# Kernel optimization log

Hardware: AMD Instinct MI355X
Metric: run time of the kernel (lower is better)

Reference implementation:

```python
import jax, jax.numpy as jnp
import numpy as np

HEADS = 16
HEAD_DIM = 64
EMBED = HEADS * HEAD_DIM  # 1024
N, L = 4, 4096


def setup_inputs() -> dict:
    key = jax.random.key(0)
    k1, k2, k3, k4, k5, k6, k7, k8 = jax.random.split(key, 8)
    s = 0.02
    return {
        "q": jax.random.normal(k1, (N, L, EMBED), jnp.float32),
        "k": jax.random.normal(k2, (N, L, EMBED), jnp.float32),
        "v": jax.random.normal(k3, (N, L, EMBED), jnp.float32),
        "mask": jnp.ones((N, L, HEADS, HEADS), jnp.int32),
        # torch Linear weights: (out_features, in_features)
        "q_w": jax.random.normal(k4, (HEAD_DIM, HEAD_DIM), jnp.float32) * s,
        "k_w": jax.random.normal(k5, (HEAD_DIM, HEAD_DIM), jnp.float32) * s,
        "v_w": jax.random.normal(k6, (HEAD_DIM, HEAD_DIM), jnp.float32) * s,
        "fc_w": jax.random.normal(k7, (EMBED, EMBED), jnp.float32) * s,
        "fc_b": jax.random.normal(k8, (EMBED,), jnp.float32) * s,
    }


def reference(q, k, v, mask, q_w, k_w, v_w, fc_w, fc_b):
    n, ql = q.shape[0], q.shape[1]
    # reshape to (N, L, H, D) and apply per-head-dim linear projections (x @ W.T)
    q4 = q.reshape(n, ql, HEADS, HEAD_DIM) @ q_w.T
    k4 = k.reshape(n, k.shape[1], HEADS, HEAD_DIM) @ k_w.T
    v4 = v.reshape(n, v.shape[1], HEADS, HEAD_DIM) @ v_w.T
    # Faithful to the original: matmul broadcasts over (N, L), contracting head_dim,
    # so logits are (N, L, H, H) -- attention across heads per token.
    scale = 1.0 / jnp.sqrt(jnp.float32(HEAD_DIM))
    logits = jnp.einsum("nlhd,nlgd->nlhg", q4, k4) * scale
    logits = jnp.where(mask == 0, -jnp.inf, logits)
    weights = jax.nn.softmax(logits, axis=-1)
    out4 = jnp.einsum("nlhg,nlgd->nlhd", weights, v4)  # (N, L, H, D)
    # Faithful scrambled reshape: permute to (N, H, L, D) then flatten to (N, L, H*D)
    out = out4.transpose(0, 2, 1, 3).reshape(n, ql, HEADS * HEAD_DIM)
    return out @ fc_w.T + fc_b
```

## Files before the change

kernel.cpp:

```cpp
#include <hip/hip_runtime.h>
#include <hip/hip_bf16.h>
#include <stdint.h>

#define TOKENS 16384
#define LSEQ 4096
#define WPAD 72

typedef short bf16x8 __attribute__((ext_vector_type(8)));
typedef float f32x4 __attribute__((ext_vector_type(4)));

typedef __attribute__((address_space(1))) void as1_t;
typedef __attribute__((address_space(3))) void as3_t;

__device__ __forceinline__ unsigned short f2bf(float x) {
  __hip_bfloat16 t = __float2bfloat16(x);
  return *reinterpret_cast<unsigned short*>(&t);
}

__device__ __forceinline__ void async16(const void* g, void* lds) {
  __builtin_amdgcn_global_load_lds((as1_t*)const_cast<void*>(g),
                                   (as3_t*)lds, 16, 0, 0);
}

__global__ __launch_bounds__(256) void cvt_bf16(const float* __restrict__ s,
                                                unsigned short* __restrict__ d,
                                                int n4) {
  int i = blockIdx.x * 256 + threadIdx.x;
  if (i < n4) {
    float4 f = ((const float4*)s)[i];
    union { unsigned short us[4]; uint2 u2; } pk;
    pk.us[0] = f2bf(f.x); pk.us[1] = f2bf(f.y);
    pk.us[2] = f2bf(f.z); pk.us[3] = f2bf(f.w);
    ((uint2*)d)[i] = pk.u2;
  }
}

__global__ __launch_bounds__(1024) void prep_weights(
    const float* __restrict__ qw, const float* __restrict__ kw,
    const float* __restrict__ vw, unsigned short* __restrict__ Mout,
    unsigned short* __restrict__ vwout) {
  __shared__ float ql[4096], kl[4096];
  const int t = threadIdx.x;
  ((float4*)ql)[t] = ((const float4*)qw)[t];
  ((float4*)kl)[t] = ((const float4*)kw)[t];
  {
    float4 f = ((const float4*)vw)[t];
    union { unsigned short us[4]; uint2 u2; } pk;
    pk.us[0] = f2bf(f.x); pk.us[1] = f2bf(f.y);
    pk.us[2] = f2bf(f.z); pk.us[3] = f2bf(f.w);
    ((uint2*)vwout)[t] = pk.u2;
  }
  __syncthreads();
  const int f = t >> 4;
  const int e0 = (t & 15) * 4;
  float acc0 = 0.f, acc1 = 0.f, acc2 = 0.f, acc3 = 0.f;
#pragma unroll 8
  for (int d = 0; d < 64; ++d) {
    const float qv = ql[d * 64 + f];
    const float4 kv = *(const float4*)&kl[d * 64 + e0];
    acc0 += qv * kv.x; acc1 += qv * kv.y; acc2 += qv * kv.z; acc3 += qv * kv.w;
  }
  union { unsigned short us[4]; uint2 u2; } pk;
  pk.us[0] = f2bf(acc0); pk.us[1] = f2bf(acc1);
  pk.us[2] = f2bf(acc2); pk.us[3] = f2bf(acc3);
  *(uint2*)&Mout[f * 64 + e0] = pk.u2;
}

__global__ __launch_bounds__(256) void attn6(
    const float* __restrict__ q, const float* __restrict__ k,
    const float* __restrict__ v, const int* __restrict__ mask,
    const unsigned short* __restrict__ Mg, const unsigned short* __restrict__ vwg,
    unsigned short* __restrict__ X) {
  __shared__ unsigned short Ml[64 * WPAD];
  __shared__ unsigned short Vw[64 * WPAD];
  __shared__ char stg_[4][6144];
  __shared__ char scr_[4][2048];

  const int tid = threadIdx.x;
  const int l = tid & 63, w = tid >> 6;
  const int lr = l & 15, lg = l >> 4;
  char* stg = stg_[w];
  char* scr = scr_[w];

  {
    const int row = tid >> 2, c0 = (tid & 3) * 16;
    *(uint4*)&Ml[row * WPAD + c0]     = *(const uint4*)(Mg + row * 64 + c0);
    *(uint4*)&Ml[row * WPAD + c0 + 8] = *(const uint4*)(Mg + row * 64 + c0 + 8);
    *(uint4*)&Vw[row * WPAD + c0]     = *(const uint4*)(vwg + row * 64 + c0);
    *(uint4*)&Vw[row * WPAD + c0 + 8] = *(const uint4*)(vwg + row * 64 + c0 + 8);
  }

  const int tok0 = blockIdx.x * 32 + w * 8;

  float4 L[2][12];
  int4 mk[2];
  {
    const size_t tb = (size_t)tok0 * 1024;
#pragma unroll
    for (int i = 0; i < 4; ++i) {
      L[0][i]     = *(const float4*)(q + tb + i * 256 + l * 4);
      L[0][4 + i] = *(const float4*)(k + tb + i * 256 + l * 4);
      L[0][8 + i] = *(const float4*)(v + tb + i * 256 + l * 4);
    }
    mk[0] = *(const int4*)(mask + (size_t)tok0 * 256 + lr * 16 + lg * 4);
  }
  __syncthreads();

  const int fr0 = lr * 128 + ((lg * 16) ^ ((lr & 7) << 4));
  const int fr1 = lr * 128 + (((64 + lg * 16)) ^ ((lr & 7) << 4));

#pragma unroll
  for (int t = 0; t < 8; ++t) {
    const int cur = t & 1, nxt = cur ^ 1;
    const int tok = tok0 + t;

#pragma unroll
    for (int i = 0; i < 4; ++i) {
      const int row = i * 4 + (l >> 4);
      const int cb = (l & 15) * 8;
      char* base = stg + row * 128 + (cb ^ ((row & 7) << 4));
      union { unsigned short us[4]; uint2 u2; } pq, pk_, pv_;
      const float4 fq = L[cur][i], fk = L[cur][4 + i], fv = L[cur][8 + i];
      pq.us[0] = f2bf(fq.x); pq.us[1] = f2bf(fq.y); pq.us[2] = f2bf(fq.z); pq.us[3] = f2bf(fq.w);
      pk_.us[0] = f2bf(fk.x); pk_.us[1] = f2bf(fk.y); pk_.us[2] = f2bf(fk.z); pk_.us[3] = f2bf(fk.w);
      pv_.us[0] = f2bf(fv.x); pv_.us[1] = f2bf(fv.y); pv_.us[2] = f2bf(fv.z); pv_.us[3] = f2bf(fv.w);
      *(uint2*)(base)        = pq.u2;
      *(uint2*)(base + 2048) = pk_.u2;
      *(uint2*)(base + 4096) = pv_.u2;
    }

    if (t < 7) {
      const size_t tb = (size_t)(tok + 1) * 1024;
#pragma unroll
      for (int i = 0; i < 4; ++i) {
        L[nxt][i]     = *(const float4*)(q + tb + i * 256 + l * 4);
        L[nxt][4 + i] = *(const float4*)(k + tb + i * 256 + l * 4);
        L[nxt][8 + i] = *(const float4*)(v + tb + i * 256 + l * 4);
      }
      mk[nxt] = *(const int4*)(mask + (size_t)(tok + 1) * 256 + lr * 16 + lg * 4);
    }
    __builtin_amdgcn_sched_barrier(0);

    const bf16x8 aq0 = *(const bf16x8*)(stg + fr0);
    const bf16x8 aq1 = *(const bf16x8*)(stg + fr1);
    const bf16x8 ak0 = *(const bf16x8*)(stg + 2048 + fr0);
    const bf16x8 ak1 = *(const bf16x8*)(stg + 2048 + fr1);
    const bf16x8 av0 = *(const bf16x8*)(stg + 4096 + fr0);
    const bf16x8 av1 = *(const bf16x8*)(stg + 4096 + fr1);

    f32x4 accu[4], accv[4];
#pragma unroll
    for (int n = 0; n < 4; ++n) {
      const int wrow = (n * 16 + lr) * WPAD;
      f32x4 z = {};
      const bf16x8 bm0 = *(const bf16x8*)&Ml[wrow + lg * 8];
      const bf16x8 bm1 = *(const bf16x8*)&Ml[wrow + 32 + lg * 8];
      accu[n] = __builtin_amdgcn_mfma_f32_16x16x32_bf16(ak0, bm0, z, 0, 0, 0);
      accu[n] = __builtin_amdgcn_mfma_f32_16x16x32_bf16(ak1, bm1, accu[n], 0, 0, 0);
      const bf16x8 bw0 = *(const bf16x8*)&Vw[wrow + lg * 8];
      const bf16x8 bw1 = *(const bf16x8*)&Vw[wrow + 32 + lg * 8];
      accv[n] = __builtin_amdgcn_mfma_f32_16x16x32_bf16(av0, bw0, z, 0, 0, 0);
      accv[n] = __builtin_amdgcn_mfma_f32_16x16x32_bf16(av1, bw1, accv[n], 0, 0, 0);
    }

#pragma unroll
    for (int n = 0; n < 4; ++n)
#pragma unroll
      for (int r = 0; r < 4; ++r) {
        const int row = lg * 4 + r;
        *(unsigned short*)(scr + row * 128 + ((32 * n + 2 * lr) ^ ((row & 7) << 4))) =
            f2bf(accu[n][r]);
      }
    const bf16x8 ua0 = *(const bf16x8*)(scr + fr0);
    const bf16x8 ua1 = *(const bf16x8*)(scr + fr1);
    f32x4 z4 = {};
    f32x4 st = __builtin_amdgcn_mfma_f32_16x16x32_bf16(ua0, aq0, z4, 0, 0, 0);
    st = __builtin_amdgcn_mfma_f32_16x16x32_bf16(ua1, aq1, st, 0, 0, 0);

    float e[4];
    float sm = 0.f;
    const int mks[4] = {mk[cur].x, mk[cur].y, mk[cur].z, mk[cur].w};
#pragma unroll
    for (int r = 0; r < 4; ++r) {
      e[r] = (mks[r] != 0) ? __expf(st[r] * 0.125f) : 0.f;
      sm += e[r];
    }
    sm += __shfl_xor(sm, 16);
    sm += __shfl_xor(sm, 32);
    const float inv = 1.0f / sm;
#pragma unroll
    for (int r = 0; r < 4; ++r) e[r] *= inv;

    bf16x8 apv;
#pragma unroll
    for (int j = 0; j < 8; ++j) {
      const int srcg = (lg * 2 + (j >> 2)) & 3;
      const float pv = __shfl(e[j & 3], lr + srcg * 16, 64);
      apv[j] = (short)((lg < 2) ? f2bf(pv) : (unsigned short)0);
    }

    const int s0 = lr + ((lg & 1) * 2) * 16;
    const int s1 = s0 + 16;
    f32x4 o[4];
#pragma unroll
    for (int n = 0; n < 4; ++n) {
      bf16x8 bv;
#pragma unroll
      for (int j = 0; j < 8; ++j) {
        const float xv = __shfl(accv[n][j & 3], (j < 4) ? s0 : s1, 64);
        bv[j] = (short)f2bf(xv);
      }
      f32x4 z = {};
      o[n] = __builtin_amdgcn_mfma_f32_16x16x32_bf16(apv, bv, z, 0, 0, 0);
    }

#pragma unroll
    for (int n = 0; n < 4; ++n)
#pragma unroll
      for (int r = 0; r < 4; ++r) {
        const int row = lg * 4 + r;
        *(unsigned short*)(scr + row * 128 + ((32 * n + 2 * lr) ^ ((row & 7) << 4))) =
            f2bf(o[n][r]);
      }
    const int nb = tok >> 12, lpos = tok & (LSEQ - 1);
#pragma unroll
    for (int it = 0; it < 2; ++it) {
      const int idx = it * 64 + l;
      const int h = idx >> 3, c = idx & 7;
      const uint4 val = *(const uint4*)(scr + h * 128 + ((c * 16) ^ ((h & 7) << 4)));
      *(uint4*)&X[((size_t)(nb * 16 + h) * LSEQ + lpos) * 64 + c * 8] = val;
    }
  }
}

__global__ __launch_bounds__(256) void gemm_fc(const unsigned short* __restrict__ A,
                                               const unsigned short* __restrict__ B,
                                               const float* __restrict__ bias,
                                               float* __restrict__ C) {
  __shared__ unsigned short sA[128 * 32];
  __shared__ unsigned short sB[128 * 32];
  const int tid = threadIdx.x;
  const int l = tid & 63, w = tid >> 6;
  const int wr = w >> 1, wc = w & 1;

  const int bid = blockIdx.x;
  const int wg = (bid & 7) * 128 + (bid >> 3);
  const int tm = (wg >> 3) * 128;
  const int tn = (wg & 7) * 128;

  f32x4 acc[4][4] = {};

  const int r0 = w * 16 + (l >> 2);
  const int c8 = (l & 3) * 8;

  for (int kt = 0; kt < 32; ++kt) {
    const int k0 = kt * 32;
#pragma unroll
    for (int s = 0; s < 2; ++s) {
      async16(A + (size_t)(tm + s * 64 + r0) * 1024 + k0 + c8,
              (char*)sA + s * 4096 + w * 1024);
      async16(B + (size_t)(tn + s * 64 + r0) * 1024 + k0 + c8,
              (char*)sB + s * 4096 + w * 1024);
    }
    __syncthreads();

    bf16x8 af[4], bfr[4];
#pragma unroll
    for (int fi = 0; fi < 4; ++fi)
      af[fi] = *(const bf16x8*)((const char*)sA +
                                (wr * 64 + fi * 16 + (l & 15)) * 64 + (l >> 4) * 16);
#pragma unroll
    for (int fj = 0; fj < 4; ++fj)
      bfr[fj] = *(const bf16x8*)((const char*)sB +
                                 (wc * 64 + fj * 16 + (l & 15)) * 64 + (l >> 4) * 16);
#pragma unroll
    for (int fi = 0; fi < 4; ++fi)
#pragma unroll
      for (int fj = 0; fj < 4; ++fj)
        acc[fi][fj] = __builtin_amdgcn_mfma_f32_16x16x32_bf16(af[fi], bfr[fj],
                                                              acc[fi][fj], 0, 0, 0);
    __syncthreads();
  }

#pragma unroll
  for (int fj = 0; fj < 4; ++fj) {
    const int col = tn + wc * 64 + fj * 16 + (l & 15);
    const float bv = bias[col];
#pragma unroll
    for (int fi = 0; fi < 4; ++fi) {
#pragma unroll
      for (int r = 0; r < 4; ++r) {
        const int row = tm + wr * 64 + fi * 16 + (l >> 4) * 4 + r;
        C[(size_t)row * 1024 + col] = acc[fi][fj][r] + bv;
      }
    }
  }
}

extern "C" void kernel_launch(void* const* d_in, const int* in_sizes, int n_in,
                              void* d_out, int out_size, void* d_ws, size_t ws_size,
                              hipStream_t stream) {
  (void)in_sizes; (void)n_in; (void)out_size; (void)ws_size;
  const float* q   = (const float*)d_in[0];
  const float* k   = (const float*)d_in[1];
  const float* v   = (const float*)d_in[2];
  const int*  mask = (const int*)d_in[3];
  const float* qw  = (const float*)d_in[4];
  const float* kw  = (const float*)d_in[5];
  const float* vw  = (const float*)d_in[6];
  const float* fcw = (const float*)d_in[7];
  const float* fcb = (const float*)d_in[8];
  float* out = (float*)d_out;

  unsigned short* X   = (unsigned short*)d_ws;
  unsigned short* Wb  = X + (size_t)16 * 1024 * 1024;
  unsigned short* Mw  = Wb + (size_t)1024 * 1024;
  unsigned short* vwb = Mw + 4096;

  cvt_bf16<<<dim3(1024), dim3(256), 0, stream>>>(fcw, Wb, 262144);
  prep_weights<<<dim3(1), dim3(1024), 0, stream>>>(qw, kw, vw, Mw, vwb);
  attn6<<<dim3(512), dim3(256), 0, stream>>>(q, k, v, mask, Mw, vwb, X);
  gemm_fc<<<dim3(1024), dim3(256), 0, stream>>>(X, Wb, fcb, out);
}
```

Measured before the change: 116.8 us.

## Stream attention inputs via async global-to-LDS loads with double-buffered fp32 staging

```diff
diff --git a/kernel.cpp b/kernel.cpp
--- a/kernel.cpp
+++ b/kernel.cpp
@@ -15,6 +15,15 @@
 __device__ __forceinline__ unsigned short f2bf(float x) {
   __hip_bfloat16 t = __float2bfloat16(x);
   return *reinterpret_cast<unsigned short*>(&t);
+}
+
+__device__ __forceinline__ bf16x8 pack8(float4 a, float4 b) {
+  bf16x8 t;
+  t[0] = (short)f2bf(a.x); t[1] = (short)f2bf(a.y);
+  t[2] = (short)f2bf(a.z); t[3] = (short)f2bf(a.w);
+  t[4] = (short)f2bf(b.x); t[5] = (short)f2bf(b.y);
+  t[6] = (short)f2bf(b.z); t[7] = (short)f2bf(b.w);
+  return t;
 }
 
 __device__ __forceinline__ void async16(const void* g, void* lds) {
@@ -66,87 +75,76 @@
   *(uint2*)&Mout[f * 64 + e0] = pk.u2;
 }
 
-__global__ __launch_bounds__(256) void attn6(
+#define STG_BYTES 13312
+
+__global__ __launch_bounds__(128) void attn7(
     const float* __restrict__ q, const float* __restrict__ k,
     const float* __restrict__ v, const int* __restrict__ mask,
     const unsigned short* __restrict__ Mg, const unsigned short* __restrict__ vwg,
     unsigned short* __restrict__ X) {
   __shared__ unsigned short Ml[64 * WPAD];
   __shared__ unsigned short Vw[64 * WPAD];
-  __shared__ char stg_[4][6144];
-  __shared__ char scr_[4][2048];
+  __shared__ char stg_[2][2][STG_BYTES];
+  __shared__ char scr_[2][2048];
 
   const int tid = threadIdx.x;
   const int l = tid & 63, w = tid >> 6;
   const int lr = l & 15, lg = l >> 4;
-  char* stg = stg_[w];
   char* scr = scr_[w];
 
   {
-    const int row = tid >> 2, c0 = (tid & 3) * 16;
-    *(uint4*)&Ml[row * WPAD + c0]     = *(const uint4*)(Mg + row * 64 + c0);
-    *(uint4*)&Ml[row * WPAD + c0 + 8] = *(const uint4*)(Mg + row * 64 + c0 + 8);
-    *(uint4*)&Vw[row * WPAD + c0]     = *(const uint4*)(vwg + row * 64 + c0);
-    *(uint4*)&Vw[row * WPAD + c0 + 8] = *(const uint4*)(vwg + row * 64 + c0 + 8);
-  }
-
-  const int tok0 = blockIdx.x * 32 + w * 8;
-
-  float4 L[2][12];
-  int4 mk[2];
-  {
-    const size_t tb = (size_t)tok0 * 1024;
+    const int row = tid >> 1, c0 = (tid & 1) * 32;
+#pragma unroll
+    for (int j = 0; j < 4; ++j) {
+      *(uint4*)&Ml[row * WPAD + c0 + j * 8] = *(const uint4*)(Mg + row * 64 + c0 + j * 8);
+      *(uint4*)&Vw[row * WPAD + c0 + j * 8] = *(const uint4*)(vwg + row * 64 + c0 + j * 8);
+    }
+  }
+  __syncthreads();
+
+  auto issue = [&](int tok, char* dst) {
+    const size_t tb = (size_t)tok * 1024;
 #pragma unroll
     for (int i = 0; i < 4; ++i) {
-      L[0][i]     = *(const float4*)(q + tb + i * 256 + l * 4);
-      L[0][4 + i] = *(const float4*)(k + tb + i * 256 + l * 4);
-      L[0][8 + i] = *(const float4*)(v + tb + i * 256 + l * 4);
-    }
-    mk[0] = *(const int4*)(mask + (size_t)tok0 * 256 + lr * 16 + lg * 4);
-  }
-  __syncthreads();
-
-  const int fr0 = lr * 128 + ((lg * 16) ^ ((lr & 7) << 4));
-  const int fr1 = lr * 128 + (((64 + lg * 16)) ^ ((lr & 7) << 4));
+      const int r = i * 4 + (l >> 4);
+      const int se = r * 64 + (((l & 15) ^ (r & 7)) << 2);
+      async16(q + tb + se, dst + i * 1024);
+      async16(k + tb + se, dst + 4096 + i * 1024);
+      async16(v + tb + se, dst + 8192 + i * 1024);
+    }
+    async16(mask + (size_t)tok * 256 + l * 4, dst + 12288);
+  };
+
+  const int tok0 = (blockIdx.x * 2 + w) * 8;
+  issue(tok0, stg_[w][0]);
+
+  const int r7 = lr & 7;
+  const int fr0 = lr * 128 + ((lg * 16) ^ (r7 << 4));
+  const int fr1 = lr * 128 + ((64 + lg * 16) ^ (r7 << 4));
 
 #pragma unroll
   for (int t = 0; t < 8; ++t) {
-    const int cur = t & 1, nxt = cur ^ 1;
     const int tok = tok0 + t;
-
-#pragma unroll
-    for (int i = 0; i < 4; ++i) {
-      const int row = i * 4 + (l >> 4);
-      const int cb = (l & 15) * 8;
-      char* base = stg + row * 128 + (cb ^ ((row & 7) << 4));
-      union { unsigned short us[4]; uint2 u2; } pq, pk_, pv_;
-      const float4 fq = L[cur][i], fk = L[cur][4 + i], fv = L[cur][8 + i];
-      pq.us[0] = f2bf(fq.x); pq.us[1] = f2bf(fq.y); pq.us[2] = f2bf(fq.z); pq.us[3] = f2bf(fq.w);
-      pk_.us[0] = f2bf(fk.x); pk_.us[1] = f2bf(fk.y); pk_.us[2] = f2bf(fk.z); pk_.us[3] = f2bf(fk.w);
-      pv_.us[0] = f2bf(fv.x); pv_.us[1] = f2bf(fv.y); pv_.us[2] = f2bf(fv.z); pv_.us[3] = f2bf(fv.w);
-      *(uint2*)(base)        = pq.u2;
-      *(uint2*)(base + 2048) = pk_.u2;
-      *(uint2*)(base + 4096) = pv_.u2;
-    }
+    char* cur = stg_[w][t & 1];
 
     if (t < 7) {
-      const size_t tb = (size_t)(tok + 1) * 1024;
-#pragma unroll
-      for (int i = 0; i < 4; ++i) {
-        L[nxt][i]     = *(const float4*)(q + tb + i * 256 + l * 4);
-        L[nxt][4 + i] = *(const float4*)(k + tb + i * 256 + l * 4);
-        L[nxt][8 + i] = *(const float4*)(v + tb + i * 256 + l * 4);
-      }
-      mk[nxt] = *(const int4*)(mask + (size_t)(tok + 1) * 256 + lr * 16 + lg * 4);
+      issue(tok + 1, stg_[w][(t + 1) & 1]);
+      asm volatile("s_waitcnt vmcnt(13)" ::: "memory");
+    } else {
+      asm volatile("s_waitcnt vmcnt(2)" ::: "memory");
     }
     __builtin_amdgcn_sched_barrier(0);
 
-    const bf16x8 aq0 = *(const bf16x8*)(stg + fr0);
-    const bf16x8 aq1 = *(const bf16x8*)(stg + fr1);
-    const bf16x8 ak0 = *(const bf16x8*)(stg + 2048 + fr0);
-    const bf16x8 ak1 = *(const bf16x8*)(stg + 2048 + fr1);
-    const bf16x8 av0 = *(const bf16x8*)(stg + 4096 + fr0);
-    const bf16x8 av1 = *(const bf16x8*)(stg + 4096 + fr1);
+    const int4 mk4 = *(const int4*)(cur + 12288 + lr * 64 + lg * 16);
+    auto ldfrag = [&](const char* base, int kc) -> bf16x8 {
+      const int c0 = kc * 8 + 2 * lg;
+      const float4 f0 = *(const float4*)(base + lr * 256 + (((c0) ^ r7) << 4));
+      const float4 f1 = *(const float4*)(base + lr * 256 + (((c0 + 1) ^ r7) << 4));
+      return pack8(f0, f1);
+    };
+    const bf16x8 aq0 = ldfrag(cur, 0),        aq1 = ldfrag(cur, 1);
+    const bf16x8 ak0 = ldfrag(cur + 4096, 0), ak1 = ldfrag(cur + 4096, 1);
+    const bf16x8 av0 = ldfrag(cur + 8192, 0), av1 = ldfrag(cur + 8192, 1);
 
     f32x4 accu[4], accv[4];
 #pragma unroll
@@ -179,7 +177,7 @@
 
     float e[4];
     float sm = 0.f;
-    const int mks[4] = {mk[cur].x, mk[cur].y, mk[cur].z, mk[cur].w};
+    const int mks[4] = {mk4.x, mk4.y, mk4.z, mk4.w};
 #pragma unroll
     for (int r = 0; r < 4; ++r) {
       e[r] = (mks[r] != 0) ? __expf(st[r] * 0.125f) : 0.f;
@@ -319,6 +317,6 @@
 
   cvt_bf16<<<dim3(1024), dim3(256), 0, stream>>>(fcw, Wb, 262144);
   prep_weights<<<dim3(1), dim3(1024), 0, stream>>>(qw, kw, vw, Mw, vwb);
-  attn6<<<dim3(512), dim3(256), 0, stream>>>(q, k, v, mask, Mw, vwb, X);
+  attn7<<<dim3(1024), dim3(128), 0, stream>>>(q, k, v, mask, Mw, vwb, X);
   gemm_fc<<<dim3(1024), dim3(256), 0, stream>>>(X, Wb, fcb, out);
 }
```

After: 120.6 us. 1.03x slower.
